# Kernel tuning notes

Measured on AMD Instinct MI355X. Metric: run time of the kernel, lower is better.

Reference implementation:

```python
import jax, jax.numpy as jnp
import numpy as np
from jax import lax

NCW = 10  # NODE_COMMAND_WIDTH
CW = 6    # COORDINATE_WIDTH
D_CMD = 512
D_COORD = 512
LATENT = 256
B, T = 64, 1024


def _lstm(x, w_ih, w_hh, b_ih, b_hh):
    """PyTorch-layout LSTM (gate order i,f,g,o). x:[B,T,D] -> h_seq:[B,T,H]."""
    H = w_hh.shape[1]
    Bx = x.shape[0]
    # precompute input projections for all timesteps: [T,B,4H]
    gates_x = (jnp.einsum('btd,gd->btg', x, w_ih) + b_ih + b_hh).transpose(1, 0, 2)

    def step(carry, gx):
        h, c = carry
        gates = gx + h @ w_hh.T
        i, f, g, o = jnp.split(gates, 4, axis=-1)
        c = jax.nn.sigmoid(f) * c + jax.nn.sigmoid(i) * jnp.tanh(g)
        h = jax.nn.sigmoid(o) * jnp.tanh(c)
        return (h, c), h

    z = jnp.zeros((Bx, H), dtype=x.dtype)
    _, h_seq = lax.scan(step, (z, z), gates_x)
    return h_seq.transpose(1, 0, 2)  # [B,T,H]


def setup_inputs() -> dict:
    key = jax.random.key(0)
    ks = jax.random.split(key, 20)
    s = 0.02
    n = lambda k, shp, sc=s: jax.random.normal(k, shp, dtype=jnp.float32) * sc
    return {
        'x': jax.random.normal(ks[0], (B, T, NCW + CW), dtype=jnp.float32),
        'context': jax.random.normal(ks[1], (B, 1, LATENT), dtype=jnp.float32),
        'w_cmd_emb': n(ks[2], (D_CMD, NCW)), 'b_cmd_emb': jnp.zeros((D_CMD,), jnp.float32),
        'w_coord_emb': n(ks[3], (D_COORD, CW)), 'b_coord_emb': jnp.zeros((D_COORD,), jnp.float32),
        'w_ih_cmd': n(ks[4], (4 * D_CMD, D_CMD + LATENT)), 'w_hh_cmd': n(ks[5], (4 * D_CMD, D_CMD)),
        'b_ih_cmd': jnp.zeros((4 * D_CMD,), jnp.float32), 'b_hh_cmd': jnp.zeros((4 * D_CMD,), jnp.float32),
        'w_ih_coord': n(ks[6], (4 * D_COORD, D_COORD + LATENT)), 'w_hh_coord': n(ks[7], (4 * D_COORD, D_COORD)),
        'b_ih_coord': jnp.zeros((4 * D_COORD,), jnp.float32), 'b_hh_coord': jnp.zeros((4 * D_COORD,), jnp.float32),
        'w_out_cmd': n(ks[8], (NCW, D_CMD)), 'b_out_cmd': jnp.zeros((NCW,), jnp.float32),
        'w_out_coord': n(ks[9], (CW, D_COORD + NCW)), 'b_out_coord': jnp.zeros((CW,), jnp.float32),
        'coord_output_scale': jnp.asarray(0.1, dtype=jnp.float32),
    }


def reference(x, context, w_cmd_emb, b_cmd_emb, w_coord_emb, b_coord_emb,
              w_ih_cmd, w_hh_cmd, b_ih_cmd, b_hh_cmd,
              w_ih_coord, w_hh_coord, b_ih_coord, b_hh_coord,
              w_out_cmd, b_out_cmd, w_out_coord, b_out_coord, coord_output_scale):
    cmd_in = x[:, :, :NCW]
    coord_in = x[:, :, NCW:]
    cmd_emb = cmd_in @ w_cmd_emb.T + b_cmd_emb      # [B,T,D_CMD]
    coord_emb = coord_in @ w_coord_emb.T + b_coord_emb  # [B,T,D_COORD]
    # dropout is identity in eval mode
    ctx = jnp.broadcast_to(context, (x.shape[0], x.shape[1], context.shape[-1]))
    x_cmd = jnp.concatenate([cmd_emb, ctx], axis=-1)
    x_coord = jnp.concatenate([coord_emb, ctx], axis=-1)
    h_cmd = _lstm(x_cmd, w_ih_cmd, w_hh_cmd, b_ih_cmd, b_hh_cmd)
    h_coord = _lstm(x_coord, w_ih_coord, w_hh_coord, b_ih_coord, b_hh_coord)
    command_output = h_cmd @ w_out_cmd.T + b_out_cmd  # [B,T,NCW]
    coord_head = jnp.concatenate([h_coord, command_output], axis=-1)
    coord_output = jnp.tanh((coord_head @ w_out_coord.T + b_out_coord) * coord_output_scale)
    return (command_output, coord_output)
```

## Files before the change

kernel.cpp:

```cpp
#include <hip/hip_runtime.h>
#include <hip/hip_bf16.h>
#include <math.h>

#define TSTEPS 1024

typedef __attribute__((ext_vector_type(8))) short short8;
typedef __attribute__((ext_vector_type(4))) float f32x4;
typedef __attribute__((ext_vector_type(4))) unsigned u32x4;

#define WS_BAR     0
#define WS_WEFF_C  1024
#define WS_WEFF_X  (WS_WEFF_C + 20480)
#define WS_BIAS_C  (WS_WEFF_X + 12288)
#define WS_BIAS_X  (WS_BIAS_C + 131072)
#define WS_HRING   (WS_BIAS_X + 131072)
#define WS_WPACK   (WS_HRING + 524288)
#define WS_WHEAD   (WS_WPACK + 2097152)

__device__ __forceinline__ float sigm(float v) { return 1.f / (1.f + __expf(-v)); }

__device__ __forceinline__ void bar_lds() {
    asm volatile("s_waitcnt lgkmcnt(0)\n\ts_barrier" ::: "memory");
}

__global__ void setup_weff_bias(const float* __restrict__ ctx,
                                const float* __restrict__ we_c, const float* __restrict__ be_c,
                                const float* __restrict__ we_x, const float* __restrict__ be_x,
                                const float* __restrict__ wih_c, const float* __restrict__ bih_c, const float* __restrict__ bhh_c,
                                const float* __restrict__ wih_x, const float* __restrict__ bih_x, const float* __restrict__ bhh_x,
                                float* __restrict__ weff_c_o, float* __restrict__ weff_x_o,
                                float* __restrict__ biasE_c_o, float* __restrict__ biasE_x_o)
{
    const int g = blockIdx.x;
    const int lstm = blockIdx.y;
    const int tid = threadIdx.x;
    const float* wih  = lstm ? wih_x : wih_c;
    const float* wemb = lstm ? we_x  : we_c;
    const float* bemb = lstm ? be_x  : be_c;
    const int NW = lstm ? 6 : 10;
    float* weff  = lstm ? weff_x_o  : weff_c_o;
    float* biasE = lstm ? biasE_x_o : biasE_c_o;
    const float* wg_ = wih + (size_t)g * 768;

    __shared__ float s_bias0;

    if (tid < NW) {
        float s = 0.f;
        for (int d = 0; d < 512; ++d) s = fmaf(wg_[d], wemb[d * NW + tid], s);
        weff[g * NW + tid] = s;
    }
    if (tid >= 64 && tid < 128) {
        int l = tid - 64;
        float s = 0.f;
        for (int i = 0; i < 8; ++i) { int d = l + i * 64; s = fmaf(wg_[d], bemb[d], s); }
        for (int m = 1; m < 64; m <<= 1) s += __shfl_xor(s, m);
        if (l == 0) s_bias0 = s;
    }
    __syncthreads();
    if (tid >= 128 && tid < 192) {
        int b = tid - 128;
        float s = s_bias0 + (lstm ? (bih_x[g] + bhh_x[g]) : (bih_c[g] + bhh_c[g]));
        const float* cb = ctx + b * 256;
        const float* wc = wg_ + 512;
        for (int c = 0; c < 256; ++c) s = fmaf(wc[c], cb[c], s);
        biasE[b * 2048 + g] = s;
    }
}

__global__ void setup_wpackF(const float* __restrict__ whh_c, const float* __restrict__ whh_x,
                             short* __restrict__ wpackF)
{
    int idx = blockIdx.x * 256 + threadIdx.x;
    int pos = idx & 511;
    int lane = pos >> 3, j = pos & 7;
    int kt4 = (idx >> 9) & 3;
    int q   = (idx >> 11) & 3;
    int wv  = (idx >> 13) & 3;
    int ub  = (idx >> 15) & 31;
    int lstm = (idx >> 20) & 1;
    int g = q * 512 + ub * 16 + (lane & 15);
    int k = wv * 128 + kt4 * 32 + (lane >> 4) * 8 + j;
    const float* whh = lstm ? whh_x : whh_c;
    float v = whh[(size_t)g * 512 + k];
    __hip_bfloat16 hi = __float2bfloat16(v);
    __hip_bfloat16 lo = __float2bfloat16(v - __bfloat162float(hi));
    size_t base = (size_t)(idx >> 9) * 1024 + pos;
    wpackF[base]       = __builtin_bit_cast(short, hi);
    wpackF[base + 512] = __builtin_bit_cast(short, lo);
}

__global__ void setup_wheadF(const float* __restrict__ w_out_cmd,
                             const float* __restrict__ w_out_coord,
                             short* __restrict__ wheadF)
{
    int idx = blockIdx.x * 256 + threadIdx.x;
    int lstm = idx >> 13;
    int rest = idx & 8191;
    int wv = rest >> 11;
    int k4 = (rest >> 9) & 3;
    int pos = rest & 511;
    int lane = pos >> 3, jj = pos & 7;
    int j = lane & 15;
    int k = wv * 128 + k4 * 32 + (lane >> 4) * 8 + jj;
    int NJ = lstm ? 6 : 10;
    float v = 0.f;
    if (j < NJ) v = lstm ? w_out_coord[(size_t)j * 522 + k] : w_out_cmd[(size_t)j * 512 + k];
    wheadF[idx] = __builtin_bit_cast(short, __float2bfloat16(v));
}

__global__ __launch_bounds__(256, 2) void lstm_main(
    const float* __restrict__ x,
    const short* __restrict__ wpackF,
    const short* __restrict__ wheadF,
    const float* __restrict__ weff_c, const float* __restrict__ weff_x,
    const float* __restrict__ biasE_c, const float* __restrict__ biasE_x,
    unsigned* __restrict__ ring,
    const float* __restrict__ b_out_cmd, const float* __restrict__ b_out_coord,
    float* __restrict__ pre_coord,
    float* __restrict__ out)
{
    __shared__ float lds_gp[4][4][16][17];
    __shared__ float lds_hp[4][16][17];
    __shared__ float x_lds[16][10];
    __shared__ float weff_lds[4][16][10];
    __shared__ short whd_lds[4][4][512];

    const int tid = threadIdx.x;
    const int bid = blockIdx.x;
    const int lane = tid & 63;
    const int wv = tid >> 6;
    const int lstm = bid >> 7;
    const int ub = (bid >> 2) & 31;
    const int bt = bid & 3;
    const int island = lstm * 4 + bt;
    const int u0 = ub * 16, b0 = bt * 16;
    const int NW = lstm ? 6 : 10;
    const int xoff = lstm ? 10 : 0;
    const int u_l = tid & 15, b_l = tid >> 4;

    const float* weff  = lstm ? weff_x : weff_c;
    const float* biasE = lstm ? biasE_x : biasE_c;

    unsigned* ring_isl = ring + island * 8 * 8192;

    const short* wb = wpackF + (size_t)(((lstm * 32 + ub) * 4 + wv) * 16) * 1024 + lane * 8;
    short8 W[4][4][2];
#pragma unroll
    for (int q = 0; q < 4; ++q)
#pragma unroll
        for (int k4 = 0; k4 < 4; ++k4) {
            W[q][k4][0] = *(const short8*)(wb + (q * 4 + k4) * 1024);
            W[q][k4][1] = *(const short8*)(wb + (q * 4 + k4) * 1024 + 512);
        }

    float biasr[4];
#pragma unroll
    for (int q = 0; q < 4; ++q)
        biasr[q] = biasE[(size_t)(b0 + b_l) * 2048 + q * 512 + u0 + u_l];

    for (int i = tid; i < 64 * NW; i += 256) {
        int r = i / NW, j = i - r * NW;
        weff_lds[r >> 4][r & 15][j] = weff[(size_t)((r >> 4) * 512 + u0 + (r & 15)) * NW + j];
    }

    float hbias = 0.f;
    const int NJ = lstm ? 6 : 10;
    if (ub == 0) {
        if (u_l < NJ) hbias = lstm ? b_out_coord[u_l] : b_out_cmd[u_l];
        const short* src = wheadF + lstm * 8192;
        short* dst = &whd_lds[0][0][0];
        for (int i = tid; i < 8192; i += 256) dst[i] = src[i];
    }

    float c_reg = 0.f;
    __syncthreads();

    for (int t = 0; t <= TSTEPS; ++t) {
        const bool last = (t == TSTEPS);
        if (last && ub != 0) break;

        float xv = 0.f;
        int xb = 0, xj = 0;
        const bool hasx = !last && (tid < 16 * NW);
        if (hasx) {
            xb = tid / NW; xj = tid - xb * NW;
            xv = x[(size_t)((b0 + xb) * TSTEPS + t) * 16 + xoff + xj];
        }

        short8 Ah[4], Al[4];
        if (t > 0) {
            const unsigned rtag = 1u + (((unsigned)(t - 1) >> 3) & 1u);
            const unsigned* rb = ring_isl + ((t + 7) & 7) * 8192 + lane * 8;
            const unsigned* p0 = rb + (wv * 4 + 0) * 512;
            const unsigned* p1 = rb + (wv * 4 + 1) * 512;
            const unsigned* p2 = rb + (wv * 4 + 2) * 512;
            const unsigned* p3 = rb + (wv * 4 + 3) * 512;
            u32x4 r0, r1, r2, r3, r4, r5, r6, r7;
            while (true) {
                asm volatile(
                    "global_load_dwordx4 %0, %8, off sc0 sc1\n\t"
                    "global_load_dwordx4 %1, %8, off offset:16 sc0 sc1\n\t"
                    "global_load_dwordx4 %2, %9, off sc0 sc1\n\t"
                    "global_load_dwordx4 %3, %9, off offset:16 sc0 sc1\n\t"
                    "global_load_dwordx4 %4, %10, off sc0 sc1\n\t"
                    "global_load_dwordx4 %5, %10, off offset:16 sc0 sc1\n\t"
                    "global_load_dwordx4 %6, %11, off sc0 sc1\n\t"
                    "global_load_dwordx4 %7, %11, off offset:16 sc0 sc1\n\t"
                    "s_waitcnt vmcnt(0)"
                    : "=&v"(r0), "=&v"(r1), "=&v"(r2), "=&v"(r3),
                      "=&v"(r4), "=&v"(r5), "=&v"(r6), "=&v"(r7)
                    : "v"(p0), "v"(p1), "v"(p2), "v"(p3)
                    : "memory");
                bool ok = true;
#pragma unroll
                for (int e = 0; e < 4; ++e) {
                    ok = ok && (((r0[e] >> 16) & 3u) == rtag) && (((r1[e] >> 16) & 3u) == rtag)
                            && (((r2[e] >> 16) & 3u) == rtag) && (((r3[e] >> 16) & 3u) == rtag)
                            && (((r4[e] >> 16) & 3u) == rtag) && (((r5[e] >> 16) & 3u) == rtag)
                            && (((r6[e] >> 16) & 3u) == rtag) && (((r7[e] >> 16) & 3u) == rtag);
                }
                if (__all((int)ok)) break;
            }
            unsigned uu[4][8];
#pragma unroll
            for (int e = 0; e < 4; ++e) {
                uu[0][e] = r0[e]; uu[0][4 + e] = r1[e];
                uu[1][e] = r2[e]; uu[1][4 + e] = r3[e];
                uu[2][e] = r4[e]; uu[2][4 + e] = r5[e];
                uu[3][e] = r6[e]; uu[3][4 + e] = r7[e];
            }
#pragma unroll
            for (int i = 0; i < 4; ++i) {
                union { unsigned u[4]; short8 s; } ah, al;
                ah.u[0] = __builtin_amdgcn_perm(uu[i][1], uu[i][0], 0x05040100u);
                ah.u[1] = __builtin_amdgcn_perm(uu[i][3], uu[i][2], 0x05040100u);
                ah.u[2] = __builtin_amdgcn_perm(uu[i][5], uu[i][4], 0x05040100u);
                ah.u[3] = __builtin_amdgcn_perm(uu[i][7], uu[i][6], 0x05040100u);
                al.u[0] = __builtin_amdgcn_perm(uu[i][1], uu[i][0], 0x07060302u);
                al.u[1] = __builtin_amdgcn_perm(uu[i][3], uu[i][2], 0x07060302u);
                al.u[2] = __builtin_amdgcn_perm(uu[i][5], uu[i][4], 0x07060302u);
                al.u[3] = __builtin_amdgcn_perm(uu[i][7], uu[i][6], 0x07060302u);
                Ah[i] = ah.s;
                Al[i] = al.s;
            }
        }

        if (!last) {
            f32x4 C[4];
#pragma unroll
            for (int q = 0; q < 4; ++q) { C[q][0] = 0.f; C[q][1] = 0.f; C[q][2] = 0.f; C[q][3] = 0.f; }
            if (t > 0) {
#pragma unroll
                for (int q = 0; q < 4; ++q)
#pragma unroll
                    for (int i = 0; i < 4; ++i) {
                        C[q] = __builtin_amdgcn_mfma_f32_16x16x32_bf16(Ah[i], W[q][i][0], C[q], 0, 0, 0);
                        C[q] = __builtin_amdgcn_mfma_f32_16x16x32_bf16(Al[i], W[q][i][0], C[q], 0, 0, 0);
                        C[q] = __builtin_amdgcn_mfma_f32_16x16x32_bf16(Ah[i], W[q][i][1], C[q], 0, 0, 0);
                    }
            }
#pragma unroll
            for (int q = 0; q < 4; ++q)
#pragma unroll
                for (int i = 0; i < 4; ++i)
                    lds_gp[wv][q][(lane >> 4) * 4 + i][lane & 15] = C[q][i];
        }

        if (ub == 0 && t > 0) {
            short8 Whd[4];
#pragma unroll
            for (int i = 0; i < 4; ++i)
                Whd[i] = *(const short8*)&whd_lds[wv][i][lane * 8];
            f32x4 Ch; Ch[0] = 0.f; Ch[1] = 0.f; Ch[2] = 0.f; Ch[3] = 0.f;
#pragma unroll
            for (int i = 0; i < 4; ++i)
                Ch = __builtin_amdgcn_mfma_f32_16x16x32_bf16(Ah[i], Whd[i], Ch, 0, 0, 0);
#pragma unroll
            for (int i = 0; i < 4; ++i)
                lds_hp[wv][(lane >> 4) * 4 + i][lane & 15] = Ch[i];
        }

        if (hasx) x_lds[xb][xj] = xv;
        bar_lds();

        if (!last) {
            float g4[4];
#pragma unroll
            for (int q = 0; q < 4; ++q) {
                float s = biasr[q];
                s += lds_gp[0][q][b_l][u_l] + lds_gp[1][q][b_l][u_l]
                   + lds_gp[2][q][b_l][u_l] + lds_gp[3][q][b_l][u_l];
                for (int j = 0; j < NW; ++j)
                    s = fmaf(weff_lds[q][u_l][j], x_lds[b_l][j], s);
                g4[q] = s;
            }
            float iv = sigm(g4[0]);
            float fv = sigm(g4[1]);
            float gv = tanhf(g4[2]);
            float ov = sigm(g4[3]);
            c_reg = fmaf(fv, c_reg, iv * gv);
            float hv = ov * tanhf(c_reg);
            __hip_bfloat16 hh = __float2bfloat16(hv);
            __hip_bfloat16 hl = __float2bfloat16(hv - __bfloat162float(hh));
            {
                const unsigned wtag = 1u + (((unsigned)t >> 3) & 1u);
                int ug = u0 + u_l;
                int kt = ug >> 5, ko = ug & 31;
                unsigned pack = (unsigned)(unsigned short)__builtin_bit_cast(short, hh)
                              | ((unsigned)(unsigned short)__builtin_bit_cast(short, hl) << 16);
                pack = (pack & ~0x00030000u) | (wtag << 16);
                unsigned idx = (unsigned)((t & 7) * 8192 + kt * 512
                             + ((ko >> 3) * 16 + b_l) * 8 + (ko & 7));
                __hip_atomic_store(&ring_isl[idx], pack, __ATOMIC_RELAXED, __HIP_MEMORY_SCOPE_AGENT);
            }
        }

        if (ub == 0 && t > 0 && u_l < NJ) {
            float hs = lds_hp[0][b_l][u_l] + lds_hp[1][b_l][u_l]
                     + lds_hp[2][b_l][u_l] + lds_hp[3][b_l][u_l] + hbias;
            const int tc = t - 1;
            if (lstm == 0)
                out[(size_t)((b0 + b_l) * TSTEPS + tc) * 10 + u_l] = hs;
            else
                pre_coord[(size_t)((b0 + b_l) * TSTEPS + tc) * 6 + u_l] = hs;
        }

        bar_lds();
    }
}

__global__ void coord_post(const float* __restrict__ w_oc,
                           const float* __restrict__ scale_p, float* __restrict__ out)
{
    int idx = blockIdx.x * 256 + threadIdx.x;
    if (idx >= 64 * TSTEPS * 6) return;
    int j = idx % 6, bt_ = idx / 6;
    float s = out[64 * TSTEPS * 10 + idx];
    const float* cmd = out + (size_t)bt_ * 10;
#pragma unroll
    for (int i = 0; i < 10; ++i) s = fmaf(cmd[i], w_oc[j * 522 + 512 + i], s);
    out[64 * TSTEPS * 10 + idx] = tanhf(s * scale_p[0]);
}

extern "C" void kernel_launch(void* const* d_in, const int* in_sizes, int n_in,
                              void* d_out, int out_size, void* d_ws, size_t ws_size,
                              hipStream_t stream)
{
    const float* x            = (const float*)d_in[0];
    const float* context      = (const float*)d_in[1];
    const float* w_cmd_emb    = (const float*)d_in[2];
    const float* b_cmd_emb    = (const float*)d_in[3];
    const float* w_coord_emb  = (const float*)d_in[4];
    const float* b_coord_emb  = (const float*)d_in[5];
    const float* w_ih_cmd     = (const float*)d_in[6];
    const float* w_hh_cmd     = (const float*)d_in[7];
    const float* b_ih_cmd     = (const float*)d_in[8];
    const float* b_hh_cmd     = (const float*)d_in[9];
    const float* w_ih_coord   = (const float*)d_in[10];
    const float* w_hh_coord   = (const float*)d_in[11];
    const float* b_ih_coord   = (const float*)d_in[12];
    const float* b_hh_coord   = (const float*)d_in[13];
    const float* w_out_cmd    = (const float*)d_in[14];
    const float* b_out_cmd    = (const float*)d_in[15];
    const float* w_out_coord  = (const float*)d_in[16];
    const float* b_out_coord  = (const float*)d_in[17];
    const float* scale        = (const float*)d_in[18];

    float* ws  = (float*)d_ws;
    float* out = (float*)d_out;

    float* weff_c   = ws + WS_WEFF_C;
    float* weff_x   = ws + WS_WEFF_X;
    float* biasE_c  = ws + WS_BIAS_C;
    float* biasE_x  = ws + WS_BIAS_X;
    unsigned* ring  = (unsigned*)(ws + WS_HRING);
    short* wpackF   = (short*)(ws + WS_WPACK);
    short* wheadF   = (short*)(ws + WS_WHEAD);
    float* pre      = out + 64 * TSTEPS * 10;

    hipMemsetAsync(ring, 0, 8 * 8 * 8192 * sizeof(unsigned), stream);

    setup_weff_bias<<<dim3(2048, 2), 256, 0, stream>>>(
        context, w_cmd_emb, b_cmd_emb, w_coord_emb, b_coord_emb,
        w_ih_cmd, b_ih_cmd, b_hh_cmd,
        w_ih_coord, b_ih_coord, b_hh_coord,
        weff_c, weff_x, biasE_c, biasE_x);

    setup_wpackF<<<8192, 256, 0, stream>>>(w_hh_cmd, w_hh_coord, wpackF);
    setup_wheadF<<<64, 256, 0, stream>>>(w_out_cmd, w_out_coord, wheadF);

    void* args[] = {
        (void*)&x, (void*)&wpackF, (void*)&wheadF,
        (void*)&weff_c, (void*)&weff_x,
        (void*)&biasE_c, (void*)&biasE_x,
        (void*)&ring,
        (void*)&b_out_cmd, (void*)&b_out_coord,
        (void*)&pre, (void*)&out
    };
    hipError_t ce = hipLaunchCooperativeKernel((const void*)lstm_main, dim3(256), dim3(256),
                                               args, 0, stream);
    if (ce != hipSuccess) {
        lstm_main<<<dim3(256), dim3(256), 0, stream>>>(
            x, wpackF, wheadF, weff_c, weff_x, biasE_c, biasE_x, ring,
            b_out_cmd, b_out_coord, pre, out);
    }

    coord_post<<<1536, 256, 0, stream>>>(w_out_coord, scale, out);
}
```

Measured before the change: 3.718 ms.

## Halve LSTM grid: each block owns 32 hidden units, rotate head projection across blocks

Each block of the persistent cooperative LSTM kernel now computes two 16-unit slices (32 hidden units) instead of one, so the grid shrinks from 256 to 128 blocks and launch bounds drop to one block per CU. Weight fragments for both halves stay in registers, so register pressure doubles. The output-head projection, previously always done by unit-block 0, now rotates across unit blocks each timestep to spread that extra work. The aim is fewer blocks taking part in the cross-block ring handoff, at the cost of twice the MFMA and gate work per block per step.

```diff
diff --git a/kernel.cpp b/kernel.cpp
--- a/kernel.cpp
+++ b/kernel.cpp
@@ -108,7 +108,7 @@
     wheadF[idx] = __builtin_bit_cast(short, __float2bfloat16(v));
 }
 
-__global__ __launch_bounds__(256, 2) void lstm_main(
+__global__ __launch_bounds__(256, 1) void lstm_main(
     const float* __restrict__ x,
     const short* __restrict__ wpackF,
     const short* __restrict__ wheadF,
@@ -119,21 +119,21 @@
     float* __restrict__ pre_coord,
     float* __restrict__ out)
 {
-    __shared__ float lds_gp[4][4][16][17];
+    __shared__ float lds_gp[2][4][4][16][17];
     __shared__ float lds_hp[4][16][17];
     __shared__ float x_lds[16][10];
-    __shared__ float weff_lds[4][16][10];
+    __shared__ float weff_lds[4][32][10];
     __shared__ short whd_lds[4][4][512];
 
     const int tid = threadIdx.x;
     const int bid = blockIdx.x;
     const int lane = tid & 63;
     const int wv = tid >> 6;
-    const int lstm = bid >> 7;
-    const int ub = (bid >> 2) & 31;
+    const int lstm = bid >> 6;
+    const int ub = (bid >> 2) & 15;
     const int bt = bid & 3;
     const int island = lstm * 4 + bt;
-    const int u0 = ub * 16, b0 = bt * 16;
+    const int u0 = ub * 32, b0 = bt * 16;
     const int NW = lstm ? 6 : 10;
     const int xoff = lstm ? 10 : 0;
     const int u_l = tid & 15, b_l = tid >> 4;
@@ -143,41 +143,47 @@
 
     unsigned* ring_isl = ring + island * 8 * 8192;
 
-    const short* wb = wpackF + (size_t)(((lstm * 32 + ub) * 4 + wv) * 16) * 1024 + lane * 8;
-    short8 W[4][4][2];
-#pragma unroll
-    for (int q = 0; q < 4; ++q)
-#pragma unroll
-        for (int k4 = 0; k4 < 4; ++k4) {
-            W[q][k4][0] = *(const short8*)(wb + (q * 4 + k4) * 1024);
-            W[q][k4][1] = *(const short8*)(wb + (q * 4 + k4) * 1024 + 512);
-        }
-
-    float biasr[4];
-#pragma unroll
-    for (int q = 0; q < 4; ++q)
-        biasr[q] = biasE[(size_t)(b0 + b_l) * 2048 + q * 512 + u0 + u_l];
-
-    for (int i = tid; i < 64 * NW; i += 256) {
+    short8 W[2][4][4][2];
+#pragma unroll
+    for (int hf = 0; hf < 2; ++hf) {
+        const short* wbh = wpackF + (size_t)(((lstm * 32 + ub * 2 + hf) * 4 + wv) * 16) * 1024 + lane * 8;
+#pragma unroll
+        for (int q = 0; q < 4; ++q)
+#pragma unroll
+            for (int k4 = 0; k4 < 4; ++k4) {
+                W[hf][q][k4][0] = *(const short8*)(wbh + (q * 4 + k4) * 1024);
+                W[hf][q][k4][1] = *(const short8*)(wbh + (q * 4 + k4) * 1024 + 512);
+            }
+    }
+
+    float biasr[2][4];
+#pragma unroll
+    for (int hf = 0; hf < 2; ++hf)
+#pragma unroll
+        for (int q = 0; q < 4; ++q)
+            biasr[hf][q] = biasE[(size_t)(b0 + b_l) * 2048 + q * 512 + u0 + hf * 16 + u_l];
+
+    for (int i = tid; i < 128 * NW; i += 256) {
         int r = i / NW, j = i - r * NW;
-        weff_lds[r >> 4][r & 15][j] = weff[(size_t)((r >> 4) * 512 + u0 + (r & 15)) * NW + j];
+        int q = r >> 5, u = r & 31;
+        weff_lds[q][u][j] = weff[(size_t)(q * 512 + u0 + u) * NW + j];
     }
 
     float hbias = 0.f;
     const int NJ = lstm ? 6 : 10;
-    if (ub == 0) {
-        if (u_l < NJ) hbias = lstm ? b_out_coord[u_l] : b_out_cmd[u_l];
+    if (u_l < NJ) hbias = lstm ? b_out_coord[u_l] : b_out_cmd[u_l];
+    {
         const short* src = wheadF + lstm * 8192;
         short* dst = &whd_lds[0][0][0];
         for (int i = tid; i < 8192; i += 256) dst[i] = src[i];
     }
 
-    float c_reg = 0.f;
+    float c_reg[2] = {0.f, 0.f};
     __syncthreads();
 
     for (int t = 0; t <= TSTEPS; ++t) {
         const bool last = (t == TSTEPS);
-        if (last && ub != 0) break;
+        if (last && ub != 15) break;
 
         float xv = 0.f;
         int xb = 0, xj = 0;
@@ -246,27 +252,35 @@
         }
 
         if (!last) {
-            f32x4 C[4];
-#pragma unroll
-            for (int q = 0; q < 4; ++q) { C[q][0] = 0.f; C[q][1] = 0.f; C[q][2] = 0.f; C[q][3] = 0.f; }
+            f32x4 C[2][4];
+#pragma unroll
+            for (int hf = 0; hf < 2; ++hf)
+#pragma unroll
+                for (int q = 0; q < 4; ++q) { C[hf][q][0] = 0.f; C[hf][q][1] = 0.f; C[hf][q][2] = 0.f; C[hf][q][3] = 0.f; }
             if (t > 0) {
 #pragma unroll
+                for (int hf = 0; hf < 2; ++hf)
+#pragma unroll
+                    for (int q = 0; q < 4; ++q)
+#pragma unroll
+                        for (int i = 0; i < 4; ++i) {
+                            C[hf][q] = __builtin_amdgcn_mfma_f32_16x16x32_bf16(Ah[i], W[hf][q][i][0], C[hf][q], 0, 0, 0);
+                            C[hf][q] = __builtin_amdgcn_mfma_f32_16x16x32_bf16(Al[i], W[hf][q][i][0], C[hf][q], 0, 0, 0);
+                            C[hf][q] = __builtin_amdgcn_mfma_f32_16x16x32_bf16(Ah[i], W[hf][q][i][1], C[hf][q], 0, 0, 0);
+                        }
+            }
+#pragma unroll
+            for (int hf = 0; hf < 2; ++hf)
+#pragma unroll
                 for (int q = 0; q < 4; ++q)
 #pragma unroll
-                    for (int i = 0; i < 4; ++i) {
-                        C[q] = __builtin_amdgcn_mfma_f32_16x16x32_bf16(Ah[i], W[q][i][0], C[q], 0, 0, 0);
-                        C[q] = __builtin_amdgcn_mfma_f32_16x16x32_bf16(Al[i], W[q][i][0], C[q], 0, 0, 0);
-                        C[q] = __builtin_amdgcn_mfma_f32_16x16x32_bf16(Ah[i], W[q][i][1], C[q], 0, 0, 0);
-                    }
-            }
-#pragma unroll
-            for (int q = 0; q < 4; ++q)
-#pragma unroll
-                for (int i = 0; i < 4; ++i)
-                    lds_gp[wv][q][(lane >> 4) * 4 + i][lane & 15] = C[q][i];
-        }
-
-        if (ub == 0 && t > 0) {
+                    for (int i = 0; i < 4; ++i)
+                        lds_gp[hf][wv][q][(lane >> 4) * 4 + i][lane & 15] = C[hf][q][i];
+            if (hasx) x_lds[xb][xj] = xv;
+        }
+
+        const bool hd = (t > 0) && (ub == ((t - 1) & 15));
+        if (hd) {
             short8 Whd[4];
 #pragma unroll
             for (int i = 0; i < 4; ++i)
@@ -279,43 +293,42 @@
             for (int i = 0; i < 4; ++i)
                 lds_hp[wv][(lane >> 4) * 4 + i][lane & 15] = Ch[i];
         }
-
-        if (hasx) x_lds[xb][xj] = xv;
         bar_lds();
 
         if (!last) {
-            float g4[4];
-#pragma unroll
-            for (int q = 0; q < 4; ++q) {
-                float s = biasr[q];
-                s += lds_gp[0][q][b_l][u_l] + lds_gp[1][q][b_l][u_l]
-                   + lds_gp[2][q][b_l][u_l] + lds_gp[3][q][b_l][u_l];
-                for (int j = 0; j < NW; ++j)
-                    s = fmaf(weff_lds[q][u_l][j], x_lds[b_l][j], s);
-                g4[q] = s;
-            }
-            float iv = sigm(g4[0]);
-            float fv = sigm(g4[1]);
-            float gv = tanhf(g4[2]);
-            float ov = sigm(g4[3]);
-            c_reg = fmaf(fv, c_reg, iv * gv);
-            float hv = ov * tanhf(c_reg);
-            __hip_bfloat16 hh = __float2bfloat16(hv);
-            __hip_bfloat16 hl = __float2bfloat16(hv - __bfloat162float(hh));
-            {
-                const unsigned wtag = 1u + (((unsigned)t >> 3) & 1u);
-                int ug = u0 + u_l;
-                int kt = ug >> 5, ko = ug & 31;
+            const unsigned wtag = 1u + (((unsigned)t >> 3) & 1u);
+#pragma unroll
+            for (int hf = 0; hf < 2; ++hf) {
+                float g4[4];
+#pragma unroll
+                for (int q = 0; q < 4; ++q) {
+                    float s = biasr[hf][q];
+                    s += lds_gp[hf][0][q][b_l][u_l] + lds_gp[hf][1][q][b_l][u_l]
+                       + lds_gp[hf][2][q][b_l][u_l] + lds_gp[hf][3][q][b_l][u_l];
+                    for (int j = 0; j < NW; ++j)
+                        s = fmaf(weff_lds[q][hf * 16 + u_l][j], x_lds[b_l][j], s);
+                    g4[q] = s;
+                }
+                float iv = sigm(g4[0]);
+                float fv = sigm(g4[1]);
+                float gv = tanhf(g4[2]);
+                float ov = sigm(g4[3]);
+                c_reg[hf] = fmaf(fv, c_reg[hf], iv * gv);
+                float hv = ov * tanhf(c_reg[hf]);
+                __hip_bfloat16 hh = __float2bfloat16(hv);
+                __hip_bfloat16 hl = __float2bfloat16(hv - __bfloat162float(hh));
                 unsigned pack = (unsigned)(unsigned short)__builtin_bit_cast(short, hh)
                               | ((unsigned)(unsigned short)__builtin_bit_cast(short, hl) << 16);
                 pack = (pack & ~0x00030000u) | (wtag << 16);
+                int ug = u0 + hf * 16 + u_l;
+                int kt = ug >> 5, ko = ug & 31;
                 unsigned idx = (unsigned)((t & 7) * 8192 + kt * 512
                              + ((ko >> 3) * 16 + b_l) * 8 + (ko & 7));
                 __hip_atomic_store(&ring_isl[idx], pack, __ATOMIC_RELAXED, __HIP_MEMORY_SCOPE_AGENT);
             }
         }
 
-        if (ub == 0 && t > 0 && u_l < NJ) {
+        if (hd && u_l < NJ) {
             float hs = lds_hp[0][b_l][u_l] + lds_hp[1][b_l][u_l]
                      + lds_hp[2][b_l][u_l] + lds_hp[3][b_l][u_l] + hbias;
             const int tc = t - 1;
@@ -397,10 +410,10 @@
         (void*)&b_out_cmd, (void*)&b_out_coord,
         (void*)&pre, (void*)&out
     };
-    hipError_t ce = hipLaunchCooperativeKernel((const void*)lstm_main, dim3(256), dim3(256),
+    hipError_t ce = hipLaunchCooperativeKernel((const void*)lstm_main, dim3(128), dim3(256),
                                                args, 0, stream);
     if (ce != hipSuccess) {
-        lstm_main<<<dim3(256), dim3(256), 0, stream>>>(
+        lstm_main<<<dim3(128), dim3(256), 0, stream>>>(
             x, wpackF, wheadF, weff_c, weff_x, biasE_c, biasE_x, ring,
             b_out_cmd, b_out_coord, pre, out);
     }
```

Result: slower. 5.697 ms (+53.2%).
